# Kernel tuning notes

Hardware: AMD Instinct MI355X
Metric: run time of the kernel (lower is better)

Reference implementation:

```python
import jax, jax.numpy as jnp
import numpy as np

B, S, D, F, E, CAP = 4, 2048, 1024, 4096, 8, 320


def setup_inputs() -> dict:
    key = jax.random.key(0)
    k1, k2, k3, k4 = jax.random.split(key, 4)
    return {
        "hidden_states": jax.random.normal(k1, (B, S, D), dtype=jnp.float32),
        "router_w": jax.random.normal(k2, (D, E), dtype=jnp.float32) * 0.02,
        "wi": jax.random.normal(k3, (E, D, F), dtype=jnp.float32) * 0.02,
        "wo": jax.random.normal(k4, (E, F, D), dtype=jnp.float32) * 0.02,
    }


def reference(hidden_states, router_w, wi, wo):
    # ---- Router (Switch top-1 with per-sequence expert capacity) ----
    b, s, d = hidden_states.shape
    e = router_w.shape[1]
    logits = hidden_states.astype(jnp.float32) @ router_w          # [B,S,E]
    probs = jax.nn.softmax(logits, axis=-1)                        # [B,S,E]
    expert_idx = jnp.argmax(probs, axis=-1)                        # [B,S]
    onehot = jax.nn.one_hot(expert_idx, e, dtype=jnp.int32)        # [B,S,E]
    priority = jnp.cumsum(onehot, axis=1)                          # cumsum over seq dim (dim=-2)
    keep = onehot * (priority <= CAP).astype(jnp.int32)            # capacity-masked router_mask

    # slot of each token within its chosen expert (0-based)
    slot = jnp.take_along_axis(priority, expert_idx[..., None], axis=-1)[..., 0] - 1  # [B,S]
    valid = slot < CAP                                             # dropped tokens exceed capacity
    slot_sc = jnp.where(valid, slot, CAP)                          # out-of-range -> dropped by scatter

    b_ar = jnp.broadcast_to(jnp.arange(b)[:, None], (b, s))
    s_ar = jnp.broadcast_to(jnp.arange(s)[None, :], (b, s))
    dispatch = jnp.zeros((b, e, CAP), jnp.int32).at[b_ar, expert_idx, slot_sc].set(
        s_ar.astype(jnp.int32), mode="drop")                       # [B,E,CAP] token index per slot
    slot_used = jnp.zeros((b, e, CAP), bool).at[b_ar, expert_idx, slot_sc].set(
        valid, mode="drop")                                        # [B,E,CAP]

    # ---- Dispatch: gather tokens into [B,E,CAP,D] ----
    xg = jax.vmap(lambda xb, ib: xb[ib])(hidden_states, dispatch)  # [B,E,CAP,D]

    # ---- Per-expert dense FFN (grouped GEMM) ----
    hg = jax.nn.relu(jnp.einsum("becd,edf->becf", xg, wi))         # [B,E,CAP,F]
    yg = jnp.einsum("becf,efd->becd", hg, wo)                      # [B,E,CAP,D]

    # ---- Combine: scatter expert outputs back; unrouted tokens keep input ----
    idx_back = jnp.where(slot_used, dispatch, s)                   # out-of-range -> dropped
    next_states = jax.vmap(
        lambda xb, ib, yb: xb.at[ib.reshape(-1)].set(yb.reshape(-1, d), mode="drop")
    )(hidden_states, idx_back, yg)                                 # [B,S,D]

    max_prob = jnp.max(probs, axis=-1, keepdims=True)              # [B,S,1]
    out = max_prob * next_states
    expert_index_out = jnp.argmax(keep, axis=-1)                   # [B,S] (0 for dropped tokens)
    return out, logits, expert_index_out
```

## Files before the change

### kernel.cpp

```cpp
#include <hip/hip_runtime.h>
#include <hip/hip_bf16.h>
#include <stdint.h>

#define B_ 4
#define S_ 2048
#define D_ 1024
#define F_ 4096
#define E_ 8
#define CAP_ 320
#define BS_ (B_*S_)
#define MPE 1280

typedef unsigned short u16;
typedef __attribute__((ext_vector_type(8))) short bf16x8;
typedef __attribute__((ext_vector_type(4))) float f32x4;
typedef __attribute__((ext_vector_type(4))) unsigned short u16x4;
typedef __attribute__((ext_vector_type(8))) unsigned short u16x8;

__device__ __forceinline__ u16 f2bf(float f) {
  union { float f; uint32_t u; } v; v.f = f;
  uint32_t r = (v.u + 0x7FFFu + ((v.u >> 16) & 1u)) >> 16;
  return (u16)r;
}

__device__ __forceinline__ void gload16(const void* g, void* l) {
  __builtin_amdgcn_global_load_lds(
      (const __attribute__((address_space(1))) uint32_t*)g,
      (__attribute__((address_space(3))) uint32_t*)l, 16, 0, 0);
}

__device__ __forceinline__ void transpose_block(
    const float* __restrict__ W, u16* __restrict__ WT,
    const int K, const int N, const int bid, void* ldsraw)
{
  float (*tile)[65] = (float(*)[65])ldsraw;
  const int tk = K >> 7, tn = N >> 6;
  const int e = bid / (tk * tn), r = bid % (tk * tn);
  const int k0 = (r / tn) << 7, n0 = (r % tn) << 6;
  const float* We = W + (size_t)e * K * N;
  u16* WTe = WT + (size_t)e * N * K;
  const int t = threadIdx.x;
  const int fr = t >> 2, c0 = (t & 3) * 16;
#pragma unroll
  for (int j = 0; j < 4; ++j) {
    const float4 v = *(const float4*)(We + (size_t)(k0 + fr) * N + n0 + c0 + j * 4);
    tile[fr][c0 + j*4 + 0] = v.x; tile[fr][c0 + j*4 + 1] = v.y;
    tile[fr][c0 + j*4 + 2] = v.z; tile[fr][c0 + j*4 + 3] = v.w;
  }
  __syncthreads();
  const int nr = t >> 3, kk0 = (t & 7) * 16;
  u16x8 o0, o1;
#pragma unroll
  for (int j = 0; j < 8; ++j) o0[j] = f2bf(tile[kk0 + j][nr]);
#pragma unroll
  for (int j = 0; j < 8; ++j) o1[j] = f2bf(tile[kk0 + 8 + j][nr]);
  u16* dst = WTe + (size_t)(n0 + nr) * K + k0 + kk0;
  *(u16x8*)dst = o0;
  *(u16x8*)(dst + 8) = o1;
}

__global__ __launch_bounds__(512) void transpose_kernel(
    const float* __restrict__ W, u16* __restrict__ WT, const int K, const int N)
{
  __shared__ __align__(16) float tile[128][65];
  transpose_block(W, WT, K, N, blockIdx.x, (void*)tile);
}

__global__ __launch_bounds__(512) void prep_kernel(
    const float* __restrict__ hs, const float* __restrict__ rw,
    const float* __restrict__ wi, u16* __restrict__ wT,
    float* __restrict__ logits, float* __restrict__ maxp,
    int* __restrict__ eidx, const int twiT)
{
  __shared__ __align__(16) float tile[128][65];
  if ((int)blockIdx.x < twiT) {
    transpose_block(wi, wT, D_, F_, blockIdx.x, (void*)tile);
    return;
  }
  const int wv = threadIdx.x >> 6, l = threadIdx.x & 63;
  const int token = (blockIdx.x - twiT) * 8 + wv;
  const float* row = hs + (size_t)token * D_;
  const float4* rw4 = (const float4*)rw;

  double acc0=0, acc1=0, acc2=0, acc3=0, acc4=0, acc5=0, acc6=0, acc7=0;
#pragma unroll
  for (int j = 0; j < 4; ++j) {
    const int d4 = l + j * 64;
    const float4 v = ((const float4*)row)[d4];
#pragma unroll
    for (int c = 0; c < 4; ++c) {
      const int d = d4 * 4 + c;
      const float x = (&v.x)[c];
      const float4 w0 = rw4[d * 2];
      const float4 w1 = rw4[d * 2 + 1];
      acc0 += (double)x * (double)w0.x;
      acc1 += (double)x * (double)w0.y;
      acc2 += (double)x * (double)w0.z;
      acc3 += (double)x * (double)w0.w;
      acc4 += (double)x * (double)w1.x;
      acc5 += (double)x * (double)w1.y;
      acc6 += (double)x * (double)w1.z;
      acc7 += (double)x * (double)w1.w;
    }
  }
  double acc[E_] = {acc0, acc1, acc2, acc3, acc4, acc5, acc6, acc7};
#pragma unroll
  for (int e = 0; e < E_; ++e) {
#pragma unroll
    for (int off = 32; off; off >>= 1)
      acc[e] += __shfl_xor(acc[e], off);
  }
  if (l == 0) {
    float lg[E_];
#pragma unroll
    for (int e = 0; e < E_; ++e) lg[e] = (float)acc[e];
    float lmax = lg[0]; int am = 0;
#pragma unroll
    for (int e = 1; e < E_; ++e) { if (lg[e] > lmax) { lmax = lg[e]; am = e; } }
    float sum = 0.f;
#pragma unroll
    for (int e = 0; e < E_; ++e) sum += expf(lg[e] - lmax);
#pragma unroll
    for (int e = 0; e < E_; ++e) logits[(size_t)token * E_ + e] = lg[e];
    maxp[token] = 1.0f / sum;
    eidx[token] = am;
  }
}

__global__ __launch_bounds__(256) void scan_kernel(
    const int* __restrict__ eidx, int* __restrict__ tok,
    float* __restrict__ eout, const float* __restrict__ hs,
    const float* __restrict__ maxp, float* __restrict__ out)
{
  const int b = blockIdx.x >> 3, e = blockIdx.x & 7;
  __shared__ int wsum[4];
  const int tid = threadIdx.x, wv = tid >> 6, l = tid & 63;
  for (int i = tid; i < CAP_; i += 256) tok[(b * E_ + e) * CAP_ + i] = -1;
  __syncthreads();
  int base = 0;
  for (int ch = 0; ch < S_ / 256; ++ch) {
    const int s = ch * 256 + tid;
    const bool p = (eidx[b * S_ + s] == e);
    const unsigned long long m = __ballot(p);
    const int lp = __popcll(m & ((1ULL << l) - 1ULL));
    if (l == 0) wsum[wv] = __popcll(m);
    __syncthreads();
    int pre = 0, tot = 0;
#pragma unroll
    for (int w = 0; w < 4; ++w) { if (w < wv) pre += wsum[w]; tot += wsum[w]; }
    if (p) {
      const int rank = base + pre + lp;
      if (rank < CAP_) {
        tok[(b * E_ + e) * CAP_ + rank] = s;
        eout[b * S_ + s] = (float)e;
      } else {
        eout[b * S_ + s] = 0.0f;
        const float mp = maxp[b * S_ + s];
        const float4* src = (const float4*)(hs + (size_t)(b * S_ + s) * D_);
        float4* dst = (float4*)(out + (size_t)(b * S_ + s) * D_);
        for (int j = 0; j < D_ / 4; ++j) {
          const float4 vv = src[j];
          float4 o; o.x = vv.x * mp; o.y = vv.y * mp; o.z = vv.z * mp; o.w = vv.w * mp;
          dst[j] = o;
        }
      }
    }
    base += tot;
    __syncthreads();
  }
}

__global__ __launch_bounds__(256) void gather_kernel(
    const float* __restrict__ hs, const int* __restrict__ tok,
    u16* __restrict__ Xg)
{
  const int bx = blockIdx.x;
  const int e = bx / MPE, r = bx % MPE;
  const int b = r / CAP_, c = r % CAP_;
  const int t = tok[(b * E_ + e) * CAP_ + c];
  const int d = threadIdx.x * 4;
  u16x4 o;
  if (t >= 0) {
    const float4 vv = *(const float4*)(hs + ((size_t)(b * S_ + t)) * D_ + d);
    o[0] = f2bf(vv.x); o[1] = f2bf(vv.y); o[2] = f2bf(vv.z); o[3] = f2bf(vv.w);
  } else {
    o[0] = 0; o[1] = 0; o[2] = 0; o[3] = 0;
  }
  *(u16x4*)(Xg + (size_t)bx * D_ + d) = o;
}

template<int MODE>
__global__ __launch_bounds__(512, 2) void moe_gemm8(
    const u16* __restrict__ Aall, const u16* __restrict__ Btall,
    u16* __restrict__ hgout, float* __restrict__ out,
    const int* __restrict__ tok, const float* __restrict__ maxp,
    const int K, const int ntn, const int gemm_blocks,
    const float* __restrict__ Wtr, u16* __restrict__ WTtr,
    const int tK, const int tN)
{
  __shared__ __align__(16) u16 lds[2][2][2][8192];

  if ((int)blockIdx.x >= gemm_blocks) {
    transpose_block(Wtr, WTtr, tK, tN, blockIdx.x - gemm_blocks, (void*)lds);
    return;
  }

  const int cpx = gemm_blocks >> 3;
  const int bid = blockIdx.x;
  const int swzb = (bid & 7) * cpx + (bid >> 3);
  const int bpe = 5 * ntn;
  const int e = swzb / bpe, rem = swzb % bpe;
  const int m0 = (rem / ntn) * 256, n0 = (rem % ntn) * 256;
  const int N = ntn * 256;

  const u16* Ae = Aall + (size_t)e * MPE * K;
  const u16* Be = Btall + (size_t)e * N * K;

  const int tid = threadIdx.x;
  const int wv = tid >> 6, l = tid & 63;
  const int wr = wv >> 2, wc = wv & 3;
  const int lr = l & 15, lk = l >> 4;
  const int rswz = ((lr >> 3) & 1) << 4;
  const int gs0 = tid ^ (((tid >> 5) & 1) << 1);
  const size_t goff = (size_t)((gs0 >> 2) & 127) * K + (size_t)((gs0 & 3) * 8);
  const int dwoff = wv * 512;

  const u16* pA0 = Ae + (size_t)m0 * K;
  const u16* pA1 = Ae + (size_t)(m0 + 128) * K;
  const u16* pB0 = Be + (size_t)n0 * K;
  const u16* pB1 = Be + (size_t)(n0 + 128) * K;

  const int NT = K >> 6;

  f32x4 acc[8][4];
#pragma unroll
  for (int i = 0; i < 8; ++i)
#pragma unroll
    for (int j = 0; j < 4; ++j) acc[i][j] = (f32x4){0.f, 0.f, 0.f, 0.f};

  bf16x8 fa[8], fb0[4], fb1[4];

#define LDSH(p, ab, h) (&lds[p][ab][h][0])

#define STAGE(dhalf, rb, tt) do {                                          \
    const u16* s_ = (rb) + goff + (size_t)((tt) * 64);                     \
    gload16(s_,      (dhalf) + dwoff);                                     \
    gload16(s_ + 32, (dhalf) + 4096 + dwoff);                              \
  } while (0)

#define READ_A(msub, p) do {                                               \
    _Pragma("unroll")                                                      \
    for (int mf = 0; mf < 4; ++mf)                                         \
      _Pragma("unroll")                                                    \
      for (int kk = 0; kk < 2; ++kk)                                       \
        fa[mf*2+kk] = *(const bf16x8*)&lds[p][0][wr]                       \
            [(kk*128 + (msub)*64 + mf*16 + lr)*32 + ((lk*8) ^ rswz)];      \
  } while (0)

#define READ_B(nsub, p, fb) do {                                           \
    _Pragma("unroll")                                                      \
    for (int nf = 0; nf < 2; ++nf)                                         \
      _Pragma("unroll")                                                    \
      for (int kk = 0; kk < 2; ++kk)                                       \
        fb[nf*2+kk] = *(const bf16x8*)&lds[p][1][wc>>1]                    \
            [(kk*128 + (wc&1)*64 + (nsub)*32 + nf*16 + lr)*32              \
             + ((lk*8) ^ rswz)];                                           \
  } while (0)

#define MFMA_Q(msub, nsub, fb) do {                                        \
    __builtin_amdgcn_s_setprio(1);                                         \
    _Pragma("unroll")                                                      \
    for (int mf = 0; mf < 4; ++mf)                                         \
      _Pragma("unroll")                                                    \
      for (int nf = 0; nf < 2; ++nf)                                       \
        _Pragma("unroll")                                                  \
        for (int kk = 0; kk < 2; ++kk)                                     \
          acc[(msub)*4+mf][(nsub)*2+nf] =                                  \
              __builtin_amdgcn_mfma_f32_16x16x32_bf16(                     \
                  fa[mf*2+kk], fb[nf*2+kk],                                \
                  acc[(msub)*4+mf][(nsub)*2+nf], 0, 0, 0);                 \
    __builtin_amdgcn_s_setprio(0);                                         \
  } while (0)

#define BAR() __builtin_amdgcn_s_barrier()
#define LGKM0() do { asm volatile("s_waitcnt lgkmcnt(0)" ::: "memory");    \
                     __builtin_amdgcn_sched_barrier(0); } while (0)
#define VM6() asm volatile("s_waitcnt vmcnt(6)" ::: "memory")
#define VM0() asm volatile("s_waitcnt vmcnt(0)" ::: "memory")

#define DO_TILE(p, pn, tc) do {                                            \
                                                                   \
    READ_A(0, p); READ_B(0, p, fb0);                                       \
    if ((tc) + 1 < NT) STAGE(LDSH(pn, 0, 1), pA1, (tc) + 1);               \
    BAR(); LGKM0();                                                        \
    MFMA_Q(0, 0, fb0);                                                     \
    BAR();                                                                 \
                                                                   \
    READ_B(1, p, fb1);                                                     \
    BAR(); LGKM0();                                                        \
    MFMA_Q(0, 1, fb1);                                                     \
    BAR();                                                                 \
                                                                   \
    READ_A(1, p);                                                          \
    if ((tc) + 2 < NT) STAGE(LDSH(p, 1, 0), pB0, (tc) + 2);                \
    BAR(); LGKM0();                                                        \
    MFMA_Q(1, 0, fb0);                                                     \
    BAR();                                                                 \
                                                                   \
    if ((tc) + 2 < NT) {                                                   \
      STAGE(LDSH(p, 1, 1), pB1, (tc) + 2);                                 \
      STAGE(LDSH(p, 0, 0), pA0, (tc) + 2);                                 \
    }                                                                      \
    BAR();                                                                 \
    MFMA_Q(1, 1, fb1);                                                     \
    if ((tc) >= NT - 2) VM0(); else VM6();                                 \
    BAR();                                                                 \
  } while (0)

  STAGE(LDSH(0, 0, 0), pA0, 0);
  STAGE(LDSH(0, 0, 1), pA1, 0);
  STAGE(LDSH(0, 1, 0), pB0, 0);
  STAGE(LDSH(0, 1, 1), pB1, 0);
  STAGE(LDSH(1, 0, 0), pA0, 1);
  STAGE(LDSH(1, 1, 0), pB0, 1);
  STAGE(LDSH(1, 1, 1), pB1, 1);
  VM6(); BAR();

  for (int t = 0; t < NT; t += 2) {
    DO_TILE(0, 1, t);
    DO_TILE(1, 0, t + 1);
  }

  if (MODE == 1) {
#pragma unroll
    for (int i = 0; i < 8; ++i) {
#pragma unroll
      for (int r = 0; r < 4; ++r) {
        const int grow = m0 + wr * 128 + i * 16 + lk * 4 + r;
        u16* hrow = hgout + ((size_t)e * MPE + grow) * (size_t)N + n0 + wc * 64;
#pragma unroll
        for (int j = 0; j < 4; ++j)
          hrow[j * 16 + lr] = f2bf(fmaxf(acc[i][j][r], 0.0f));
      }
    }
  } else {
#pragma unroll
    for (int i = 0; i < 8; ++i) {
#pragma unroll
      for (int r = 0; r < 4; ++r) {
        const int grow = m0 + wr * 128 + i * 16 + lk * 4 + r;
        const int b = grow / CAP_, c = grow % CAP_;
        const int t = tok[(b * E_ + e) * CAP_ + c];
        if (t >= 0) {
          const float sc = maxp[b * S_ + t];
          float* orow = out + ((size_t)(b * S_ + t)) * D_ + n0 + wc * 64;
#pragma unroll
          for (int j = 0; j < 4; ++j)
            orow[j * 16 + lr] = sc * acc[i][j][r];
        }
      }
    }
  }
#undef LDSH
#undef STAGE
#undef READ_A
#undef READ_B
#undef MFMA_Q
#undef BAR
#undef LGKM0
#undef VM6
#undef VM0
#undef DO_TILE
}

extern "C" void kernel_launch(void* const* d_in, const int* in_sizes, int n_in,
                              void* d_out, int out_size, void* d_ws, size_t ws_size,
                              hipStream_t stream)
{
  const float* hs = (const float*)d_in[0];
  const float* rw = (const float*)d_in[1];
  const float* wi = (const float*)d_in[2];
  const float* wo = (const float*)d_in[3];

  float* out    = (float*)d_out;
  float* logits = out + (size_t)BS_ * D_;
  float* eout   = logits + (size_t)BS_ * E_;

  uint8_t* ws = (uint8_t*)d_ws;
  int*   tok  = (int*)(ws + 0);
  float* maxp = (float*)(ws + 40960);
  int*   eidx = (int*)(ws + 73728);
  u16*   Xg   = (u16*)(ws + 131072);
  u16*   hg   = (u16*)(ws + 21102592);
  u16*   wiT  = (u16*)(ws + 104988672);
  if (ws_size < 172097536ULL) return;
  const bool big = ws_size >= 239206400ULL;
  u16* woT = big ? (u16*)(ws + 172097536) : wiT;

  const int twiT = E_ * (D_ / 128) * (F_ / 64);
  const int twoT = E_ * (F_ / 128) * (D_ / 64);
  const int g1 = E_ * 5 * (F_ / 256);
  const int g2 = E_ * 5 * (D_ / 256);

  prep_kernel<<<twiT + BS_ / 8, 512, 0, stream>>>(
      hs, rw, wi, wiT, logits, maxp, eidx, twiT);
  scan_kernel<<<B_ * E_, 256, 0, stream>>>(eidx, tok, eout, hs, maxp, out);
  gather_kernel<<<E_ * MPE, 256, 0, stream>>>(hs, tok, Xg);

  if (big) {
    moe_gemm8<1><<<g1 + twoT, 512, 0, stream>>>(
        Xg, wiT, hg, nullptr, tok, maxp, D_, F_ / 256, g1, wo, woT, F_, D_);
  } else {
    moe_gemm8<1><<<g1, 512, 0, stream>>>(
        Xg, wiT, hg, nullptr, tok, maxp, D_, F_ / 256, g1,
        nullptr, nullptr, 0, 0);
    transpose_kernel<<<twoT, 512, 0, stream>>>(wo, woT, F_, D_);
  }
  moe_gemm8<2><<<g2, 512, 0, stream>>>(
      hg, woT, nullptr, out, tok, maxp, F_, D_ / 256, g2,
      nullptr, nullptr, 0, 0);
}
```

Before: 343.9 us.

## Use 128x256 tiles for first expert GEMM to double block count

Splits the templated grouped GEMM into two specialised kernels. The first (up-projection) GEMM now uses 128-row by 256-column tiles, so it launches 1280 blocks instead of 640, with a new A staging layout, LDS map and wait counts. The aim is better occupancy and load balance across CUs and less tail imbalance. In exchange, each B tile is reused across fewer rows, which adds global traffic and halves the MFMA work per barrier. The second GEMM keeps its 256x256 tiles but its constants are now hardcoded.

Measured after the change: 345.3 us. No clear change (+0.4%).

```diff
diff --git a/kernel.cpp b/kernel.cpp
--- a/kernel.cpp
+++ b/kernel.cpp
@@ -189,29 +189,179 @@
   *(u16x4*)(Xg + (size_t)bx * D_ + d) = o;
 }
 
-template<int MODE>
-__global__ __launch_bounds__(512, 2) void moe_gemm8(
+#define BAR() __builtin_amdgcn_s_barrier()
+#define LGKM0() do { asm volatile("s_waitcnt lgkmcnt(0)" ::: "memory");    \
+                     __builtin_amdgcn_sched_barrier(0); } while (0)
+#define VMW(n) asm volatile("s_waitcnt vmcnt(" #n ")" ::: "memory")
+
+__global__ __launch_bounds__(512, 2) void moe_g1(
     const u16* __restrict__ Aall, const u16* __restrict__ Btall,
-    u16* __restrict__ hgout, float* __restrict__ out,
-    const int* __restrict__ tok, const float* __restrict__ maxp,
-    const int K, const int ntn, const int gemm_blocks,
-    const float* __restrict__ Wtr, u16* __restrict__ WTtr,
-    const int tK, const int tN)
-{
-  __shared__ __align__(16) u16 lds[2][2][2][8192];
+    u16* __restrict__ hgout, const int gemm_blocks,
+    const float* __restrict__ Wtr, u16* __restrict__ WTtr)
+{
+  __shared__ __align__(16) u16 lds[49152];
+
+#define LDA(p, h) (lds + (p) * 8192 + (h) * 4096)
+#define LDB(p, h) (lds + 16384 + (p) * 16384 + (h) * 8192)
 
   if ((int)blockIdx.x >= gemm_blocks) {
-    transpose_block(Wtr, WTtr, tK, tN, blockIdx.x - gemm_blocks, (void*)lds);
+    transpose_block(Wtr, WTtr, F_, D_, blockIdx.x - gemm_blocks, (void*)lds);
     return;
   }
-
+  const int K = D_, NT = K >> 6, N = F_;
   const int cpx = gemm_blocks >> 3;
   const int bid = blockIdx.x;
   const int swzb = (bid & 7) * cpx + (bid >> 3);
-  const int bpe = 5 * ntn;
-  const int e = swzb / bpe, rem = swzb % bpe;
-  const int m0 = (rem / ntn) * 256, n0 = (rem % ntn) * 256;
-  const int N = ntn * 256;
+  const int e = swzb / 160, rem = swzb % 160;
+  const int m0 = (rem / 16) * 128, n0 = (rem % 16) * 256;
+
+  const u16* Ae = Aall + (size_t)e * MPE * K;
+  const u16* Be = Btall + (size_t)e * N * K;
+
+  const int tid = threadIdx.x;
+  const int wv = tid >> 6, l = tid & 63;
+  const int wr = wv >> 2, wc = wv & 3;
+  const int lr = l & 15, lk = l >> 4;
+  const int rswz = ((lr >> 3) & 1) << 4;
+  const int gs0 = tid ^ (((tid >> 5) & 1) << 1);
+  const size_t goffB = (size_t)((gs0 >> 2) & 127) * K + (size_t)((gs0 & 3) * 8);
+  const size_t goffA = (size_t)((gs0 >> 2) & 63) * K
+                     + (size_t)(((gs0 >> 8) & 1) * 32) + (size_t)((gs0 & 3) * 8);
+  const int dwoff = wv * 512;
+
+  const u16* pA0 = Ae + (size_t)m0 * K;
+  const u16* pA1 = Ae + (size_t)(m0 + 64) * K;
+  const u16* pB0 = Be + (size_t)n0 * K;
+  const u16* pB1 = Be + (size_t)(n0 + 128) * K;
+
+  f32x4 acc[4][4];
+#pragma unroll
+  for (int i = 0; i < 4; ++i)
+#pragma unroll
+    for (int j = 0; j < 4; ++j) acc[i][j] = (f32x4){0.f, 0.f, 0.f, 0.f};
+
+  bf16x8 fa[4], fb0[4], fb1[4];
+
+#define STAGE_A(dhalf, rb, tt) \
+    gload16((rb) + goffA + (size_t)((tt) * 64), (dhalf) + dwoff)
+
+#define STAGE_B(dhalf, rb, tt) do {                                        \
+    const u16* s_ = (rb) + goffB + (size_t)((tt) * 64);                    \
+    gload16(s_,      (dhalf) + dwoff);                                     \
+    gload16(s_ + 32, (dhalf) + 4096 + dwoff);                              \
+  } while (0)
+
+#define READ_A1(msub, p) do {                                              \
+    _Pragma("unroll")                                                      \
+    for (int mf = 0; mf < 2; ++mf)                                         \
+      _Pragma("unroll")                                                    \
+      for (int kk = 0; kk < 2; ++kk)                                       \
+        fa[mf*2+kk] = *(const bf16x8*)&LDA(p, wr)                          \
+            [(kk*64 + ((msub)*2+mf)*16 + lr)*32 + ((lk*8) ^ rswz)];        \
+  } while (0)
+
+#define READ_B1(nsub, p, fb) do {                                          \
+    _Pragma("unroll")                                                      \
+    for (int nf = 0; nf < 2; ++nf)                                         \
+      _Pragma("unroll")                                                    \
+      for (int kk = 0; kk < 2; ++kk)                                       \
+        fb[nf*2+kk] = *(const bf16x8*)&LDB(p, wc>>1)                       \
+            [(kk*128 + (wc&1)*64 + (nsub)*32 + nf*16 + lr)*32              \
+             + ((lk*8) ^ rswz)];                                           \
+  } while (0)
+
+#define MFMA1(msub, nsub, fb) do {                                        \
+    __builtin_amdgcn_s_setprio(1);                                         \
+    _Pragma("unroll")                                                      \
+    for (int mf = 0; mf < 2; ++mf)                                         \
+      _Pragma("unroll")                                                    \
+      for (int nf = 0; nf < 2; ++nf)                                       \
+        _Pragma("unroll")                                                  \
+        for (int kk = 0; kk < 2; ++kk)                                     \
+          acc[(msub)*2+mf][(nsub)*2+nf] =                                  \
+              __builtin_amdgcn_mfma_f32_16x16x32_bf16(                     \
+                  fa[mf*2+kk], fb[nf*2+kk],                                \
+                  acc[(msub)*2+mf][(nsub)*2+nf], 0, 0, 0);                 \
+    __builtin_amdgcn_s_setprio(0);                                         \
+  } while (0)
+
+#define DO_TILE1(p, pn, tc) do {                                           \
+                                                                   \
+    READ_A1(0, p); READ_B1(0, p, fb0);                                     \
+    if ((tc) + 1 < NT) STAGE_A(LDA(pn, 1), pA1, (tc) + 1);                 \
+    BAR(); LGKM0();                                                        \
+    MFMA1(0, 0, fb0);                                                      \
+    BAR();                                                                 \
+                                                                   \
+    READ_B1(1, p, fb1);                                                    \
+    BAR(); LGKM0();                                                        \
+    MFMA1(0, 1, fb1);                                                      \
+    BAR();                                                                 \
+                                                                   \
+    READ_A1(1, p);                                                         \
+    if ((tc) + 2 < NT) STAGE_B(LDB(p, 0), pB0, (tc) + 2);                  \
+    BAR(); LGKM0();                                                        \
+    MFMA1(1, 0, fb0);                                                      \
+    BAR();                                                                 \
+                                                                   \
+    if ((tc) + 2 < NT) {                                                   \
+      STAGE_B(LDB(p, 1), pB1, (tc) + 2);                                   \
+      STAGE_A(LDA(p, 0), pA0, (tc) + 2);                                   \
+    }                                                                      \
+    BAR();                                                                 \
+    MFMA1(1, 1, fb1);                                                      \
+    if ((tc) >= NT - 2) VMW(0); else VMW(5);                               \
+    BAR();                                                                 \
+  } while (0)
+
+  STAGE_A(LDA(0, 0), pA0, 0);
+  STAGE_A(LDA(0, 1), pA1, 0);
+  STAGE_B(LDB(0, 0), pB0, 0);
+  STAGE_B(LDB(0, 1), pB1, 0);
+  STAGE_B(LDB(1, 0), pB0, 1);
+  STAGE_B(LDB(1, 1), pB1, 1);
+  STAGE_A(LDA(1, 0), pA0, 1);
+  VMW(5); BAR();
+
+  for (int t = 0; t < NT; t += 2) {
+    DO_TILE1(0, 1, t);
+    DO_TILE1(1, 0, t + 1);
+  }
+
+#pragma unroll
+  for (int i = 0; i < 4; ++i) {
+#pragma unroll
+    for (int r = 0; r < 4; ++r) {
+      const int grow = m0 + wr * 64 + i * 16 + lk * 4 + r;
+      u16* hrow = hgout + ((size_t)e * MPE + grow) * (size_t)N + n0 + wc * 64;
+#pragma unroll
+      for (int j = 0; j < 4; ++j)
+        hrow[j * 16 + lr] = f2bf(fmaxf(acc[i][j][r], 0.0f));
+    }
+  }
+#undef LDA
+#undef LDB
+#undef STAGE_A
+#undef STAGE_B
+#undef READ_A1
+#undef READ_B1
+#undef MFMA1
+#undef DO_TILE1
+}
+
+__global__ __launch_bounds__(512, 2) void moe_g2(
+    const u16* __restrict__ Aall, const u16* __restrict__ Btall,
+    float* __restrict__ out, const int* __restrict__ tok,
+    const float* __restrict__ maxp)
+{
+  __shared__ __align__(16) u16 lds[2][2][2][8192];
+
+  const int K = F_, NT = K >> 6, N = D_;
+  const int gemm_blocks = 160, cpx = gemm_blocks >> 3;
+  const int bid = blockIdx.x;
+  const int swzb = (bid & 7) * cpx + (bid >> 3);
+  const int e = swzb / 20, rem = swzb % 20;
+  const int m0 = (rem / 4) * 256, n0 = (rem % 4) * 256;
 
   const u16* Ae = Aall + (size_t)e * MPE * K;
   const u16* Be = Btall + (size_t)e * N * K;
@@ -229,8 +379,6 @@
   const u16* pA1 = Ae + (size_t)(m0 + 128) * K;
   const u16* pB0 = Be + (size_t)n0 * K;
   const u16* pB1 = Be + (size_t)(n0 + 128) * K;
-
-  const int NT = K >> 6;
 
   f32x4 acc[8][4];
 #pragma unroll
@@ -282,38 +430,28 @@
     __builtin_amdgcn_s_setprio(0);                                         \
   } while (0)
 
-#define BAR() __builtin_amdgcn_s_barrier()
-#define LGKM0() do { asm volatile("s_waitcnt lgkmcnt(0)" ::: "memory");    \
-                     __builtin_amdgcn_sched_barrier(0); } while (0)
-#define VM6() asm volatile("s_waitcnt vmcnt(6)" ::: "memory")
-#define VM0() asm volatile("s_waitcnt vmcnt(0)" ::: "memory")
-
 #define DO_TILE(p, pn, tc) do {                                            \
-                                                                   \
     READ_A(0, p); READ_B(0, p, fb0);                                       \
     if ((tc) + 1 < NT) STAGE(LDSH(pn, 0, 1), pA1, (tc) + 1);               \
     BAR(); LGKM0();                                                        \
     MFMA_Q(0, 0, fb0);                                                     \
     BAR();                                                                 \
-                                                                   \
     READ_B(1, p, fb1);                                                     \
     BAR(); LGKM0();                                                        \
     MFMA_Q(0, 1, fb1);                                                     \
     BAR();                                                                 \
-                                                                   \
     READ_A(1, p);                                                          \
     if ((tc) + 2 < NT) STAGE(LDSH(p, 1, 0), pB0, (tc) + 2);                \
     BAR(); LGKM0();                                                        \
     MFMA_Q(1, 0, fb0);                                                     \
     BAR();                                                                 \
-                                                                   \
     if ((tc) + 2 < NT) {                                                   \
       STAGE(LDSH(p, 1, 1), pB1, (tc) + 2);                                 \
       STAGE(LDSH(p, 0, 0), pA0, (tc) + 2);                                 \
     }                                                                      \
     BAR();                                                                 \
     MFMA_Q(1, 1, fb1);                                                     \
-    if ((tc) >= NT - 2) VM0(); else VM6();                                 \
+    if ((tc) >= NT - 2) VMW(0); else VMW(6);                               \
     BAR();                                                                 \
   } while (0)
 
@@ -324,40 +462,26 @@
   STAGE(LDSH(1, 0, 0), pA0, 1);
   STAGE(LDSH(1, 1, 0), pB0, 1);
   STAGE(LDSH(1, 1, 1), pB1, 1);
-  VM6(); BAR();
+  VMW(6); BAR();
 
   for (int t = 0; t < NT; t += 2) {
     DO_TILE(0, 1, t);
     DO_TILE(1, 0, t + 1);
   }
 
-  if (MODE == 1) {
-#pragma unroll
-    for (int i = 0; i < 8; ++i) {
-#pragma unroll
-      for (int r = 0; r < 4; ++r) {
-        const int grow = m0 + wr * 128 + i * 16 + lk * 4 + r;
-        u16* hrow = hgout + ((size_t)e * MPE + grow) * (size_t)N + n0 + wc * 64;
+#pragma unroll
+  for (int i = 0; i < 8; ++i) {
+#pragma unroll
+    for (int r = 0; r < 4; ++r) {
+      const int grow = m0 + wr * 128 + i * 16 + lk * 4 + r;
+      const int b = grow / CAP_, c = grow % CAP_;
+      const int t = tok[(b * E_ + e) * CAP_ + c];
+      if (t >= 0) {
+        const float sc = maxp[b * S_ + t];
+        float* orow = out + ((size_t)(b * S_ + t)) * D_ + n0 + wc * 64;
 #pragma unroll
         for (int j = 0; j < 4; ++j)
-          hrow[j * 16 + lr] = f2bf(fmaxf(acc[i][j][r], 0.0f));
-      }
-    }
-  } else {
-#pragma unroll
-    for (int i = 0; i < 8; ++i) {
-#pragma unroll
-      for (int r = 0; r < 4; ++r) {
-        const int grow = m0 + wr * 128 + i * 16 + lk * 4 + r;
-        const int b = grow / CAP_, c = grow % CAP_;
-        const int t = tok[(b * E_ + e) * CAP_ + c];
-        if (t >= 0) {
-          const float sc = maxp[b * S_ + t];
-          float* orow = out + ((size_t)(b * S_ + t)) * D_ + n0 + wc * 64;
-#pragma unroll
-          for (int j = 0; j < 4; ++j)
-            orow[j * 16 + lr] = sc * acc[i][j][r];
-        }
+          orow[j * 16 + lr] = sc * acc[i][j][r];
       }
     }
   }
@@ -366,10 +490,6 @@
 #undef READ_A
 #undef READ_B
 #undef MFMA_Q
-#undef BAR
-#undef LGKM0
-#undef VM6
-#undef VM0
 #undef DO_TILE
 }
 
@@ -399,8 +519,8 @@
 
   const int twiT = E_ * (D_ / 128) * (F_ / 64);
   const int twoT = E_ * (F_ / 128) * (D_ / 64);
-  const int g1 = E_ * 5 * (F_ / 256);
-  const int g2 = E_ * 5 * (D_ / 256);
+  const int g1 = E_ * (MPE / 128) * (F_ / 256);
+  const int g2 = 160;
 
   prep_kernel<<<twiT + BS_ / 8, 512, 0, stream>>>(
       hs, rw, wi, wiT, logits, maxp, eidx, twiT);
@@ -408,15 +528,10 @@
   gather_kernel<<<E_ * MPE, 256, 0, stream>>>(hs, tok, Xg);
 
   if (big) {
-    moe_gemm8<1><<<g1 + twoT, 512, 0, stream>>>(
-        Xg, wiT, hg, nullptr, tok, maxp, D_, F_ / 256, g1, wo, woT, F_, D_);
+    moe_g1<<<g1 + twoT, 512, 0, stream>>>(Xg, wiT, hg, g1, wo, woT);
   } else {
-    moe_gemm8<1><<<g1, 512, 0, stream>>>(
-        Xg, wiT, hg, nullptr, tok, maxp, D_, F_ / 256, g1,
-        nullptr, nullptr, 0, 0);
+    moe_g1<<<g1, 512, 0, stream>>>(Xg, wiT, hg, g1, nullptr, nullptr);
     transpose_kernel<<<twoT, 512, 0, stream>>>(wo, woT, F_, D_);
   }
-  moe_gemm8<2><<<g2, 512, 0, stream>>>(
-      hg, woT, nullptr, out, tok, maxp, F_, D_ / 256, g2,
-      nullptr, nullptr, 0, 0);
-}
+  moe_g2<<<g2, 512, 0, stream>>>(hg, woT, out, tok, maxp);
+}
```
